# Kernel optimization log

Measured on AMD Instinct MI355X. Metric: run time of the kernel, lower is better.

The kernel has to match this reference:

```python
import jax, jax.numpy as jnp
import numpy as np

B, S, D = 2, 2048, 2560
H, HKV, HD = 8, 4, 256
EPS = 1e-6
SCALING = 256 ** -0.5          # query_pre_attn_scalar ** -0.5
SOFTCAP = 4096.0               # sliding_window passed positionally into softcap slot
NEG = -1e9


def rms_norm(x, w):
    # x: [..., HD]; computed in fp32 like the torch module
    xf = x.astype(jnp.float32)
    out = xf * jax.lax.rsqrt(jnp.mean(xf * xf, axis=-1, keepdims=True) + EPS)
    return (out * (1.0 + w.astype(jnp.float32))).astype(x.dtype)


def rotate_half(x):
    x1, x2 = x[..., : HD // 2], x[..., HD // 2:]
    return jnp.concatenate((-x2, x1), axis=-1)


def apply_rope(x, cos, sin):
    # cos/sin: [B, S, HD] -> broadcast over head axis 1
    c, s = cos[:, None], sin[:, None]
    return x * c + rotate_half(x) * s


def setup_inputs() -> dict:
    key = jax.random.key(0)
    ks = jax.random.split(key, 6)
    x = jax.random.normal(ks[0], (B, S, D), dtype=jnp.float32)
    # RoPE angles (theta=10000, linear scaling factor 8)
    inv_freq = 1.0 / (10000.0 ** (np.arange(0, HD, 2, dtype=np.float32) / HD))
    pos = np.arange(S, dtype=np.float32) / 8.0
    ang = np.einsum('s,d->sd', pos, inv_freq)
    ang = np.concatenate([ang, ang], axis=-1)               # [S, HD]
    cos = jnp.asarray(np.broadcast_to(np.cos(ang), (B, S, HD)).copy())
    sin = jnp.asarray(np.broadcast_to(np.sin(ang), (B, S, HD)).copy())
    # causal additive mask [B, 1, S, S]
    causal = np.where(np.tril(np.ones((S, S), dtype=bool)), 0.0, NEG).astype(np.float32)
    mask = jnp.asarray(np.broadcast_to(causal, (B, 1, S, S)).copy())
    sc = 0.02
    q_w = jax.random.normal(ks[1], (H * HD, D), dtype=jnp.float32) * sc
    k_w = jax.random.normal(ks[2], (HKV * HD, D), dtype=jnp.float32) * sc
    v_w = jax.random.normal(ks[3], (HKV * HD, D), dtype=jnp.float32) * sc
    o_w = jax.random.normal(ks[4], (D, H * HD), dtype=jnp.float32) * sc
    qn_w = jnp.zeros((HD,), dtype=jnp.float32)
    kn_w = jnp.zeros((HD,), dtype=jnp.float32)
    return {"x": x, "cos": cos, "sin": sin, "mask": mask,
            "q_w": q_w, "k_w": k_w, "v_w": v_w, "o_w": o_w,
            "qn_w": qn_w, "kn_w": kn_w}


def reference(x, cos, sin, mask, q_w, k_w, v_w, o_w, qn_w, kn_w):
    b, s, _ = x.shape
    # projections -> [B, H(kv), S, HD]
    q = (x @ q_w.T).reshape(b, s, H, HD).transpose(0, 2, 1, 3)
    k = (x @ k_w.T).reshape(b, s, HKV, HD).transpose(0, 2, 1, 3)
    v = (x @ v_w.T).reshape(b, s, HKV, HD).transpose(0, 2, 1, 3)
    q = rms_norm(q, qn_w)
    k = rms_norm(k, kn_w)
    q = apply_rope(q, cos, sin)
    k = apply_rope(k, cos, sin)
    # GQA: repeat kv heads (interleave matches repeat_interleave on dim=1)
    rep = H // HKV
    k = jnp.repeat(k, rep, axis=1)
    v = jnp.repeat(v, rep, axis=1)
    w = jnp.einsum('bhqd,bhkd->bhqk', q, k) * SCALING
    w = jnp.tanh(w / SOFTCAP) * SOFTCAP                     # softcap (bug-faithful)
    w = w + mask[:, :, :, : k.shape[2]]
    p = jax.nn.softmax(w.astype(jnp.float32), axis=-1).astype(q.dtype)
    attn = jnp.einsum('bhqk,bhkd->bhqd', p, v)
    attn = attn.transpose(0, 2, 1, 3).reshape(b, s, H * HD)
    return attn @ o_w.T
```

## Files before the change

### kernel.cpp

```cpp
#include <hip/hip_runtime.h>
#include <hip/hip_bf16.h>

#define BB   2
#define SS   2048
#define DD   2560
#define HH   8
#define HKVV 4
#define HDD  256
#define MM   (BB*SS)
#define NQ   (HH*HDD)
#define NKV  (HKVV*HDD)
#define SCALING 0.0625f
#define SOFTCAP 4096.0f
#define CAPC    (1.0f/(3.0f*SOFTCAP*SOFTCAP))
#define M0      20.0f

typedef __attribute__((ext_vector_type(8))) short short8;
typedef __attribute__((ext_vector_type(8))) unsigned short ushort8;
typedef __attribute__((ext_vector_type(4))) unsigned short us4;
typedef __attribute__((ext_vector_type(4))) float f32x4;

__device__ __forceinline__ float bf2f(unsigned short u) {
    union { unsigned int i; float f; } v; v.i = ((unsigned int)u) << 16; return v.f;
}
__device__ __forceinline__ unsigned short f2bf(float f) {
    union { float f; unsigned int i; } v; v.f = f;
    return (unsigned short)((v.i + 0x7fffu + ((v.i >> 16) & 1u)) >> 16);
}
__device__ __forceinline__ f32x4 mfma16(short8 a, short8 b, f32x4 c) {
    return __builtin_amdgcn_mfma_f32_16x16x32_bf16(a, b, c, 0, 0, 0);
}

__device__ __forceinline__ void async_cp16(const void* g, void* l) {
    __builtin_amdgcn_global_load_lds(
        (__attribute__((address_space(1))) void*)(g),
        (__attribute__((address_space(3))) void*)(l), 16, 0, 0);
}

__device__ __forceinline__ ushort8 ld8(const unsigned short* p) { return *(const ushort8*)p; }
__device__ __forceinline__ ushort8 ld8(const float* p) {
    ushort8 r;
#pragma unroll
    for (int i = 0; i < 8; i++) r[i] = f2bf(p[i]);
    return r;
}
__device__ __forceinline__ void stc(float* p, float v)          { *p = v; }
__device__ __forceinline__ void stc(unsigned short* p, float v) { *p = f2bf(v); }
__device__ __forceinline__ void stage8(const unsigned short* src, unsigned short* lds) {
    async_cp16(src, lds);
}
__device__ __forceinline__ void stage8(const float* src, unsigned short* lds) {
    *(ushort8*)lds = ld8(src);
}

__global__ __launch_bounds__(256) void cvt_bf16(const float* __restrict__ in,
                                                unsigned short* __restrict__ out, int n4)
{
    int i = blockIdx.x * 256 + threadIdx.x;
    const int stride = gridDim.x * 256;
    for (; i < n4; i += stride) {
        float4 v = ((const float4*)in)[i];
        us4 o;
        o[0] = f2bf(v.x); o[1] = f2bf(v.y); o[2] = f2bf(v.z); o[3] = f2bf(v.w);
        ((us4*)out)[i] = o;
    }
}

template<typename TA, typename TB, typename TC, bool VT_OUT>
__global__ __launch_bounds__(256) void gemm_k(const TA* __restrict__ A,
                                              const TB* __restrict__ Bm,
                                              TC* __restrict__ C,
                                              int M, int N, int K)
{
    __shared__ __align__(16) unsigned short As[128][32];
    __shared__ __align__(16) unsigned short Bs[128][32];

    const int tid  = threadIdx.x;
    const int bm   = blockIdx.x, bn = blockIdx.y;
    const int wave = tid >> 6, lane = tid & 63;
    const int quad = lane >> 4, lm = lane & 15;
    const int wm = (wave >> 1) * 64, wn = (wave & 1) * 64;

    f32x4 acc[4][4];
#pragma unroll
    for (int i = 0; i < 4; i++)
#pragma unroll
        for (int j = 0; j < 4; j++) acc[i][j] = (f32x4)0.0f;

    unsigned short* AsF = &As[0][0];
    unsigned short* BsF = &Bs[0][0];
    const int grow = tid >> 2;
    const int gcol = (tid & 3) * 8;
    const TA* Ab = A  + (size_t)(bm * 128) * K;
    const TB* Bb = Bm + (size_t)(bn * 128) * K;

    for (int k0 = 0; k0 < K; k0 += 32) {
        stage8(&Ab[(size_t)(grow     ) * K + k0 + gcol], AsF + tid * 8);
        stage8(&Ab[(size_t)(grow + 64) * K + k0 + gcol], AsF + 2048 + tid * 8);
        stage8(&Bb[(size_t)(grow     ) * K + k0 + gcol], BsF + tid * 8);
        stage8(&Bb[(size_t)(grow + 64) * K + k0 + gcol], BsF + 2048 + tid * 8);
        __syncthreads();

        short8 af[4], bf[4];
#pragma unroll
        for (int t = 0; t < 4; t++) af[t] = *(const short8*)&As[wm + t * 16 + lm][quad * 8];
#pragma unroll
        for (int t = 0; t < 4; t++) bf[t] = *(const short8*)&Bs[wn + t * 16 + lm][quad * 8];
#pragma unroll
        for (int i = 0; i < 4; i++)
#pragma unroll
            for (int j = 0; j < 4; j++)
                acc[i][j] = mfma16(af[i], bf[j], acc[i][j]);
        __syncthreads();
    }

#pragma unroll
    for (int i = 0; i < 4; i++)
#pragma unroll
        for (int j = 0; j < 4; j++) {
            if constexpr (VT_OUT) {
                int row0 = bm * 128 + wm + i * 16 + quad * 4;
                int col  = bn * 128 + wn + j * 16 + lm;
                int b    = row0 >> 11, s0 = row0 & (SS - 1);
                int kvh  = col >> 8,   d  = col & (HDD - 1);
                us4 pk;
#pragma unroll
                for (int r = 0; r < 4; r++) pk[r] = f2bf(acc[i][j][r]);
                *(us4*)&C[(((size_t)b * HKVV + kvh) * HDD + d) * SS + s0] = pk;
            } else {
#pragma unroll
                for (int r = 0; r < 4; r++) {
                    int row = bm * 128 + wm + i * 16 + quad * 4 + r;
                    int col = bn * 128 + wn + j * 16 + lm;
                    stc(&C[(size_t)row * N + col], acc[i][j][r]);
                }
            }
        }
}

__global__ __launch_bounds__(256) void norm_rope(unsigned short* __restrict__ X,
                                                 const float* __restrict__ nw,
                                                 const float* __restrict__ cosb,
                                                 const float* __restrict__ sinb,
                                                 int nheads)
{
    const int bs = blockIdx.x;
    const int h  = blockIdx.y;
    const int t  = threadIdx.x;

    __shared__ float xs[256];
    __shared__ float red[4];

    const size_t base = ((size_t)bs * nheads + h) * HDD;
    float v = bf2f(X[base + t]);
    xs[t] = v;

    float p = v * v;
#pragma unroll
    for (int off = 32; off >= 1; off >>= 1) p += __shfl_xor(p, off);
    if ((t & 63) == 0) red[t >> 6] = p;
    __syncthreads();
    float sum = red[0] + red[1] + red[2] + red[3];
    float rs  = rsqrtf(sum * (1.0f / HDD) + 1e-6f);

    const int pt = (t + 128) & 255;
    float w1 = 1.0f + nw[t];
    float w2 = 1.0f + nw[pt];
    float normed  = v * rs * w1;
    float partner = xs[pt] * rs * w2;
    float rot = (t < 128) ? -partner : partner;
    float c = cosb[(size_t)bs * HDD + t];
    float s = sinb[(size_t)bs * HDD + t];
    X[base + t] = f2bf(normed * c + rot * s);
}

__device__ const unsigned char unit_tbl[48] = {
    62, 124, 125, 120, 121,
    58, 116, 117, 112, 113,
    54, 108, 109, 104, 105,
    50, 100, 101,  96,  97,
    46,  92,  93,  88,  89,
    42,  84,  85,  80,  81,
    38,  76,  77,  72,  73,
    34,  68,  69,  64,  65,
    30,  26,  22,  18,  14, 10, 6, 2
};

__global__ __launch_bounds__(256) void attn_split(const unsigned short* __restrict__ Q,
                                                  const unsigned short* __restrict__ K,
                                                  const unsigned short* __restrict__ VT,
                                                  unsigned short* __restrict__ O,
                                                  float* __restrict__ Opart,
                                                  float* __restrict__ lpart)
{
    const int tid = threadIdx.x, w = tid >> 6, lane = tid & 63;
    const int quad = lane >> 4, lm = lane & 15;
    const int hb = blockIdx.x;
    const int h = hb & 7, b = hb >> 3, kvh = h >> 1;

    const unsigned int u = unit_tbl[blockIdx.y];
    const int qb = u >> 2;
    const bool single = (u & 2) != 0;
    const int half = u & 1;
    const int q0 = qb * 64;
    const int T  = 2 * (qb + 1);
    const int t_lo = (!single && half) ? (qb + 1) : 0;
    const int t_hi = single ? T : (half ? T : (qb + 1));

    __shared__ __align__(16) unsigned short Ks[2][32 * 256];
    __shared__ __align__(16) unsigned short Vt[2][256 * 32];
    __shared__ __align__(16) unsigned short Ps[4 * 512];

    const unsigned short* Qb = Q + (((size_t)b * SS + q0 + w * 16 + lm) * HH + h) * HDD;
    short8 qf[8];
#pragma unroll
    for (int c = 0; c < 8; c++) qf[c] = *(const short8*)&Qb[c * 32 + quad * 8];

    const unsigned short* Kb = K  + (size_t)b * SS * NKV + (size_t)kvh * HDD;
    const unsigned short* Vb = VT + ((size_t)b * HKVV + kvh) * HDD * (size_t)SS;

    f32x4 o_acc[16];
#pragma unroll
    for (int i = 0; i < 16; i++) o_acc[i] = (f32x4)0.0f;
    float l_r[4] = {0.f, 0.f, 0.f, 0.f};

    const int mylo = q0 + w * 16;
    const int row  = mylo + quad * 4;

    auto STAGE = [&](int bi, int k0) {
#pragma unroll
        for (int p = 0; p < 4; p++) {
            const int slot = p * 256 + tid;
            const int krow = slot >> 5, kc = slot & 31;
            async_cp16(&Kb[(size_t)(k0 + krow) * NKV + ((kc ^ (krow & 7)) * 8)],
                       &Ks[bi][slot * 8]);
            const int vd = slot >> 2, vc = slot & 3;
            async_cp16(&Vb[(size_t)vd * SS + k0 + ((vc ^ ((vd >> 1) & 3)) * 8)],
                       &Vt[bi][slot * 8]);
        }
    };

    STAGE(0, t_lo * 32);
    int cur = 0;

    for (int t = t_lo; t < t_hi; t++) {
        const int k0 = t * 32;

        if (t + 1 < t_hi) {
            STAGE(cur ^ 1, k0 + 32);
            asm volatile("s_waitcnt vmcnt(8)" ::: "memory");
        } else {
            asm volatile("s_waitcnt vmcnt(0)" ::: "memory");
        }
        __builtin_amdgcn_s_barrier();
        __builtin_amdgcn_sched_barrier(0);

        if (k0 <= mylo + 15) {
            f32x4 sa0 = (f32x4)0.0f, sa1 = (f32x4)0.0f;
            __builtin_amdgcn_s_setprio(1);
#pragma unroll
            for (int c = 0; c < 8; c++) {
                const int cs = (((c * 4 + quad) ^ (lm & 7))) * 8;
                short8 kf0 = *(const short8*)&Ks[cur][lm * 256 + cs];
                short8 kf1 = *(const short8*)&Ks[cur][(16 + lm) * 256 + cs];
                sa0 = mfma16(qf[c], kf0, sa0);
                sa1 = mfma16(qf[c], kf1, sa1);
            }
            __builtin_amdgcn_s_setprio(0);

            const bool msk = (k0 + 31 > mylo);
            float pe[2][4];
#pragma unroll
            for (int t2 = 0; t2 < 2; t2++) {
                const int key = k0 + t2 * 16 + lm;
#pragma unroll
                for (int r = 0; r < 4; r++) {
                    float s = (t2 ? sa1[r] : sa0[r]) * SCALING;
                    s = s - s * s * s * CAPC;
                    float e = __expf(s - M0);
                    if (msk && key > row + r) e = 0.0f;
                    pe[t2][r] = e;
                    l_r[r] += e;
                }
            }

#pragma unroll
            for (int t2 = 0; t2 < 2; t2++)
#pragma unroll
                for (int r = 0; r < 4; r++) {
                    const int g = (t2 * 2 + (lm >> 3)) ^ r ^ quad;
                    Ps[w * 512 + (quad * 4 + r) * 32 + g * 8 + (lm & 7)] = f2bf(pe[t2][r]);
                }
            asm volatile("s_waitcnt lgkmcnt(0)" ::: "memory");
            __builtin_amdgcn_sched_barrier(0);
            const int gr = quad ^ (lm & 3) ^ (lm >> 2);
            short8 pf = *(const short8*)&Ps[w * 512 + lm * 32 + gr * 8];

            __builtin_amdgcn_s_setprio(1);
#pragma unroll
            for (int nt = 0; nt < 16; nt++) {
                short8 vf = *(const short8*)&Vt[cur][(nt * 16 + lm) * 32
                                                    + ((quad ^ ((lm >> 1) & 3)) * 8)];
                o_acc[nt] = mfma16(pf, vf, o_acc[nt]);
            }
            __builtin_amdgcn_s_setprio(0);
        }

        __builtin_amdgcn_sched_barrier(0);
        __builtin_amdgcn_s_barrier();
        __builtin_amdgcn_sched_barrier(0);
        cur ^= 1;
    }

#pragma unroll
    for (int off = 1; off < 16; off <<= 1)
#pragma unroll
        for (int r = 0; r < 4; r++) l_r[r] += __shfl_xor(l_r[r], off);

    if (single) {
#pragma unroll
        for (int r = 0; r < 4; r++) {
            float inv = 1.0f / l_r[r];
            unsigned short* Ob = O + ((size_t)b * SS + row + r) * NQ + h * HDD;
#pragma unroll
            for (int nt = 0; nt < 16; nt++)
                Ob[nt * 16 + lm] = f2bf(o_acc[nt][r] * inv);
        }
    } else {
        const int slot = (((b * HH + h) * 16 + (qb - 16)) << 1) | half;
        float* Ob = Opart + ((size_t)slot * 64 + w * 16 + quad * 4) * 256;
#pragma unroll
        for (int r = 0; r < 4; r++) {
            if (lm == 0) lpart[slot * 64 + w * 16 + quad * 4 + r] = l_r[r];
#pragma unroll
            for (int nt = 0; nt < 16; nt++)
                Ob[(size_t)r * 256 + nt * 16 + lm] = o_acc[nt][r];
        }
    }
}

__global__ __launch_bounds__(256) void attn_reduce(const float* __restrict__ Op,
                                                   const float* __restrict__ lp,
                                                   unsigned short* __restrict__ ATT)
{
    const int sp  = blockIdx.x >> 4;
    const int wr0 = (blockIdx.x & 15) * 4;
    const int r   = threadIdx.x >> 6;
    const int c0  = (threadIdx.x & 63) * 4;
    const int wrow = wr0 + r;
    const int qbm = sp & 15, h = (sp >> 4) & 7, b = sp >> 7;

    const size_t base0 = ((size_t)(sp * 2) * 64 + wrow) * 256;
    const size_t base1 = base0 + (size_t)64 * 256;
    float4 a = *(const float4*)&Op[base0 + c0];
    float4 d = *(const float4*)&Op[base1 + c0];
    float l = lp[sp * 2 * 64 + wrow] + lp[(sp * 2 + 1) * 64 + wrow];
    float inv = 1.0f / l;
    us4 o;
    o[0] = f2bf((a.x + d.x) * inv); o[1] = f2bf((a.y + d.y) * inv);
    o[2] = f2bf((a.z + d.z) * inv); o[3] = f2bf((a.w + d.w) * inv);
    const int srow = (16 + qbm) * 64 + wrow;
    *(us4*)&ATT[(((size_t)b * SS + srow) * HH + h) * HDD + c0] = o;
}

__global__ __launch_bounds__(256) void attn_kernel(const unsigned short* __restrict__ Q,
                                                   const unsigned short* __restrict__ K,
                                                   const unsigned short* __restrict__ VT,
                                                   unsigned short* __restrict__ O)
{
    const int tid = threadIdx.x, w = tid >> 6, lane = tid & 63;
    const int quad = lane >> 4, lm = lane & 15;
    const int h = blockIdx.y, b = blockIdx.z, kvh = h >> 1;

    const int bx = blockIdx.x;
    const int qb = (bx & 1) ? (31 - (bx >> 1)) : (bx >> 1);
    const int q0 = qb * 64;
    const int T  = 2 * (qb + 1);

    __shared__ __align__(16) unsigned short Ks[2][32 * 256];
    __shared__ __align__(16) unsigned short Vt[2][256 * 32];
    __shared__ __align__(16) unsigned short Ps[4 * 512];

    const unsigned short* Qb = Q + (((size_t)b * SS + q0 + w * 16 + lm) * HH + h) * HDD;
    short8 qf[8];
#pragma unroll
    for (int c = 0; c < 8; c++) qf[c] = *(const short8*)&Qb[c * 32 + quad * 8];

    const unsigned short* Kb = K  + (size_t)b * SS * NKV + (size_t)kvh * HDD;
    const unsigned short* Vb = VT + ((size_t)b * HKVV + kvh) * HDD * (size_t)SS;

    f32x4 o_acc[16];
#pragma unroll
    for (int i = 0; i < 16; i++) o_acc[i] = (f32x4)0.0f;
    float l_r[4] = {0.f, 0.f, 0.f, 0.f};

    const int mylo = q0 + w * 16;
    const int row  = mylo + quad * 4;

    auto STAGE = [&](int bi, int k0) {
#pragma unroll
        for (int p = 0; p < 4; p++) {
            const int slot = p * 256 + tid;
            const int krow = slot >> 5, kc = slot & 31;
            async_cp16(&Kb[(size_t)(k0 + krow) * NKV + ((kc ^ (krow & 7)) * 8)],
                       &Ks[bi][slot * 8]);
            const int vd = slot >> 2, vc = slot & 3;
            async_cp16(&Vb[(size_t)vd * SS + k0 + ((vc ^ ((vd >> 1) & 3)) * 8)],
                       &Vt[bi][slot * 8]);
        }
    };

    STAGE(0, 0);
    int cur = 0;

    for (int t = 0; t < T; t++) {
        const int k0 = t * 32;

        if (t + 1 < T) {
            STAGE(cur ^ 1, k0 + 32);
            asm volatile("s_waitcnt vmcnt(8)" ::: "memory");
        } else {
            asm volatile("s_waitcnt vmcnt(0)" ::: "memory");
        }
        __builtin_amdgcn_s_barrier();
        __builtin_amdgcn_sched_barrier(0);

        if (k0 <= mylo + 15) {
            f32x4 sa0 = (f32x4)0.0f, sa1 = (f32x4)0.0f;
            __builtin_amdgcn_s_setprio(1);
#pragma unroll
            for (int c = 0; c < 8; c++) {
                const int cs = (((c * 4 + quad) ^ (lm & 7))) * 8;
                short8 kf0 = *(const short8*)&Ks[cur][lm * 256 + cs];
                short8 kf1 = *(const short8*)&Ks[cur][(16 + lm) * 256 + cs];
                sa0 = mfma16(qf[c], kf0, sa0);
                sa1 = mfma16(qf[c], kf1, sa1);
            }
            __builtin_amdgcn_s_setprio(0);

            const bool msk = (k0 + 31 > mylo);
            float pe[2][4];
#pragma unroll
            for (int t2 = 0; t2 < 2; t2++) {
                const int key = k0 + t2 * 16 + lm;
#pragma unroll
                for (int r = 0; r < 4; r++) {
                    float s = (t2 ? sa1[r] : sa0[r]) * SCALING;
                    s = s - s * s * s * CAPC;
                    float e = __expf(s - M0);
                    if (msk && key > row + r) e = 0.0f;
                    pe[t2][r] = e;
                    l_r[r] += e;
                }
            }

#pragma unroll
            for (int t2 = 0; t2 < 2; t2++)
#pragma unroll
                for (int r = 0; r < 4; r++) {
                    const int g = (t2 * 2 + (lm >> 3)) ^ r ^ quad;
                    Ps[w * 512 + (quad * 4 + r) * 32 + g * 8 + (lm & 7)] = f2bf(pe[t2][r]);
                }
            asm volatile("s_waitcnt lgkmcnt(0)" ::: "memory");
            __builtin_amdgcn_sched_barrier(0);
            const int gr = quad ^ (lm & 3) ^ (lm >> 2);
            short8 pf = *(const short8*)&Ps[w * 512 + lm * 32 + gr * 8];

            __builtin_amdgcn_s_setprio(1);
#pragma unroll
            for (int nt = 0; nt < 16; nt++) {
                short8 vf = *(const short8*)&Vt[cur][(nt * 16 + lm) * 32
                                                    + ((quad ^ ((lm >> 1) & 3)) * 8)];
                o_acc[nt] = mfma16(pf, vf, o_acc[nt]);
            }
            __builtin_amdgcn_s_setprio(0);
        }

        __builtin_amdgcn_sched_barrier(0);
        __builtin_amdgcn_s_barrier();
        __builtin_amdgcn_sched_barrier(0);
        cur ^= 1;
    }

#pragma unroll
    for (int off = 1; off < 16; off <<= 1)
#pragma unroll
        for (int r = 0; r < 4; r++) l_r[r] += __shfl_xor(l_r[r], off);
#pragma unroll
    for (int r = 0; r < 4; r++) {
        float inv = 1.0f / l_r[r];
        unsigned short* Ob = O + ((size_t)b * SS + row + r) * NQ + h * HDD;
#pragma unroll
        for (int nt = 0; nt < 16; nt++)
            Ob[nt * 16 + lm] = f2bf(o_acc[nt][r] * inv);
    }
}

extern "C" void kernel_launch(void* const* d_in, const int* in_sizes, int n_in,
                              void* d_out, int out_size, void* d_ws, size_t ws_size,
                              hipStream_t stream)
{
    const float* x    = (const float*)d_in[0];
    const float* cosb = (const float*)d_in[1];
    const float* sinb = (const float*)d_in[2];
    const float* q_w  = (const float*)d_in[4];
    const float* k_w  = (const float*)d_in[5];
    const float* v_w  = (const float*)d_in[6];
    const float* o_w  = (const float*)d_in[7];
    const float* qn_w = (const float*)d_in[8];
    const float* kn_w = (const float*)d_in[9];
    float* out = (float*)d_out;

    const size_t sz_xb = (size_t)MM * DD;
    const size_t sz_wq = (size_t)NQ * DD;
    const size_t sz_wk = (size_t)NKV * DD;
    const size_t sz_q  = (size_t)MM * NQ;
    const size_t sz_k  = (size_t)MM * NKV;

    const size_t needA = (sz_xb + 2 * sz_wq + 2 * sz_wk + sz_q + 2 * sz_k) * 2;
    const size_t needB = (2 * sz_wq + 2 * sz_wk + sz_q + 2 * sz_k) * 2;

    if (ws_size >= needA) {
        unsigned short* xb  = (unsigned short*)d_ws;
        unsigned short* wqb = xb  + sz_xb;
        unsigned short* wkb = wqb + sz_wq;
        unsigned short* wvb = wkb + sz_wk;
        unsigned short* wob = wvb + sz_wk;
        unsigned short* Qw  = wob + sz_wq;
        unsigned short* Kw  = Qw  + sz_q;
        unsigned short* VTw = Kw  + sz_k;
        float* Opart = (float*)d_ws;
        float* lpart = Opart + (size_t)512 * 64 * 256;
        unsigned short* ATT = Qw;

        cvt_bf16<<<2048, 256, 0, stream>>>(x,   xb,  (int)(sz_xb / 4));
        cvt_bf16<<<2048, 256, 0, stream>>>(q_w, wqb, (int)(sz_wq / 4));
        cvt_bf16<<<1024, 256, 0, stream>>>(k_w, wkb, (int)(sz_wk / 4));
        cvt_bf16<<<1024, 256, 0, stream>>>(v_w, wvb, (int)(sz_wk / 4));
        cvt_bf16<<<2048, 256, 0, stream>>>(o_w, wob, (int)(sz_wq / 4));

        gemm_k<unsigned short, unsigned short, unsigned short, false>
            <<<dim3(MM/128, NQ /128), 256, 0, stream>>>(xb, wqb, Qw,  MM, NQ,  DD);
        gemm_k<unsigned short, unsigned short, unsigned short, false>
            <<<dim3(MM/128, NKV/128), 256, 0, stream>>>(xb, wkb, Kw,  MM, NKV, DD);
        gemm_k<unsigned short, unsigned short, unsigned short, true>
            <<<dim3(MM/128, NKV/128), 256, 0, stream>>>(xb, wvb, VTw, MM, NKV, DD);

        norm_rope<<<dim3(MM, HH),   256, 0, stream>>>(Qw, qn_w, cosb, sinb, HH);
        norm_rope<<<dim3(MM, HKVV), 256, 0, stream>>>(Kw, kn_w, cosb, sinb, HKVV);

        attn_split<<<dim3(16, 48), 256, 0, stream>>>(Qw, Kw, VTw, ATT, Opart, lpart);
        attn_reduce<<<4096, 256, 0, stream>>>(Opart, lpart, ATT);

        gemm_k<unsigned short, unsigned short, float, false>
            <<<dim3(MM/128, DD/128), 256, 0, stream>>>(ATT, wob, out, MM, DD, NQ);
    } else if (ws_size >= needB) {
        unsigned short* wqb = (unsigned short*)d_ws;
        unsigned short* wkb = wqb + sz_wq;
        unsigned short* wvb = wkb + sz_wk;
        unsigned short* wob = wvb + sz_wk;
        unsigned short* Qw  = wob + sz_wq;
        unsigned short* Kw  = Qw  + sz_q;
        unsigned short* VTw = Kw  + sz_k;
        unsigned short* ATT = wqb;

        cvt_bf16<<<2048, 256, 0, stream>>>(q_w, wqb, (int)(sz_wq / 4));
        cvt_bf16<<<1024, 256, 0, stream>>>(k_w, wkb, (int)(sz_wk / 4));
        cvt_bf16<<<1024, 256, 0, stream>>>(v_w, wvb, (int)(sz_wk / 4));
        cvt_bf16<<<2048, 256, 0, stream>>>(o_w, wob, (int)(sz_wq / 4));

        gemm_k<float, unsigned short, unsigned short, false>
            <<<dim3(MM/128, NQ /128), 256, 0, stream>>>(x, wqb, Qw,  MM, NQ,  DD);
        gemm_k<float, unsigned short, unsigned short, false>
            <<<dim3(MM/128, NKV/128), 256, 0, stream>>>(x, wkb, Kw,  MM, NKV, DD);
        gemm_k<float, unsigned short, unsigned short, true>
            <<<dim3(MM/128, NKV/128), 256, 0, stream>>>(x, wvb, VTw, MM, NKV, DD);

        norm_rope<<<dim3(MM, HH),   256, 0, stream>>>(Qw, qn_w, cosb, sinb, HH);
        norm_rope<<<dim3(MM, HKVV), 256, 0, stream>>>(Kw, kn_w, cosb, sinb, HKVV);

        attn_kernel<<<dim3(32, HH, BB), 256, 0, stream>>>(Qw, Kw, VTw, ATT);

        gemm_k<unsigned short, unsigned short, float, false>
            <<<dim3(MM/128, DD/128), 256, 0, stream>>>(ATT, wob, out, MM, DD, NQ);
    } else {
        unsigned short* Qw  = (unsigned short*)d_ws;
        unsigned short* Kw  = Qw  + sz_q;
        unsigned short* VTw = Kw  + sz_k;
        unsigned short* ATT = VTw + sz_k;

        gemm_k<float, float, unsigned short, false>
            <<<dim3(MM/128, NQ /128), 256, 0, stream>>>(x, q_w, Qw,  MM, NQ,  DD);
        gemm_k<float, float, unsigned short, false>
            <<<dim3(MM/128, NKV/128), 256, 0, stream>>>(x, k_w, Kw,  MM, NKV, DD);
        gemm_k<float, float, unsigned short, true>
            <<<dim3(MM/128, NKV/128), 256, 0, stream>>>(x, v_w, VTw, MM, NKV, DD);

        norm_rope<<<dim3(MM, HH),   256, 0, stream>>>(Qw, qn_w, cosb, sinb, HH);
        norm_rope<<<dim3(MM, HKVV), 256, 0, stream>>>(Kw, kn_w, cosb, sinb, HKVV);

        attn_kernel<<<dim3(32, HH, BB), 256, 0, stream>>>(Qw, Kw, VTw, ATT);

        gemm_k<unsigned short, float, float, false>
            <<<dim3(MM/128, DD/128), 256, 0, stream>>>(ATT, o_w, out, MM, DD, NQ);
    }
}
```

Baseline: 549.8 us.

## Single-buffer V tile in attention LDS and split K/V staging with extra barrier

The V tile moves from a double buffer to a single LDS buffer, so the attention block uses less shared memory and may fit more resident blocks per CU. K keeps its prefetch one tile ahead. V for the next tile is now issued only after the PV MFMAs finish, so its load overlaps only with the next QK^T and softmax phase. A second vmcnt wait and barrier per iteration guard the single V buffer. This adds synchronisation and exposes more V load latency in exchange for the lower LDS footprint.

```diff
diff --git a/kernel.cpp b/kernel.cpp
--- a/kernel.cpp
+++ b/kernel.cpp
@@ -208,7 +208,7 @@
     const int t_hi = single ? T : (half ? T : (qb + 1));
 
     __shared__ __align__(16) unsigned short Ks[2][32 * 256];
-    __shared__ __align__(16) unsigned short Vt[2][256 * 32];
+    __shared__ __align__(16) unsigned short Vt[256 * 32];
     __shared__ __align__(16) unsigned short Ps[4 * 512];
 
     const unsigned short* Qb = Q + (((size_t)b * SS + q0 + w * 16 + lm) * HH + h) * HDD;
@@ -227,34 +227,43 @@
     const int mylo = q0 + w * 16;
     const int row  = mylo + quad * 4;
 
-    auto STAGE = [&](int bi, int k0) {
+    auto STAGE_K = [&](int bi, int k0) {
 #pragma unroll
         for (int p = 0; p < 4; p++) {
             const int slot = p * 256 + tid;
             const int krow = slot >> 5, kc = slot & 31;
             async_cp16(&Kb[(size_t)(k0 + krow) * NKV + ((kc ^ (krow & 7)) * 8)],
                        &Ks[bi][slot * 8]);
+        }
+    };
+    auto STAGE_V = [&](int k0) {
+#pragma unroll
+        for (int p = 0; p < 4; p++) {
+            const int slot = p * 256 + tid;
             const int vd = slot >> 2, vc = slot & 3;
             async_cp16(&Vb[(size_t)vd * SS + k0 + ((vc ^ ((vd >> 1) & 3)) * 8)],
-                       &Vt[bi][slot * 8]);
+                       &Vt[slot * 8]);
         }
     };
 
-    STAGE(0, t_lo * 32);
+    STAGE_K(0, t_lo * 32);
+    STAGE_V(t_lo * 32);
     int cur = 0;
 
     for (int t = t_lo; t < t_hi; t++) {
         const int k0 = t * 32;
-
-        if (t + 1 < t_hi) {
-            STAGE(cur ^ 1, k0 + 32);
+        const bool more = (t + 1 < t_hi);
+
+        if (more) {
+            STAGE_K(cur ^ 1, k0 + 32);
             asm volatile("s_waitcnt vmcnt(8)" ::: "memory");
         } else {
-            asm volatile("s_waitcnt vmcnt(0)" ::: "memory");
+            asm volatile("s_waitcnt vmcnt(4)" ::: "memory");
         }
         __builtin_amdgcn_s_barrier();
         __builtin_amdgcn_sched_barrier(0);
 
+        short8 pf;
         if (k0 <= mylo + 15) {
             f32x4 sa0 = (f32x4)0.0f, sa1 = (f32x4)0.0f;
             __builtin_amdgcn_s_setprio(1);
@@ -294,13 +303,20 @@
             asm volatile("s_waitcnt lgkmcnt(0)" ::: "memory");
             __builtin_amdgcn_sched_barrier(0);
             const int gr = quad ^ (lm & 3) ^ (lm >> 2);
-            short8 pf = *(const short8*)&Ps[w * 512 + lm * 32 + gr * 8];
-
+            pf = *(const short8*)&Ps[w * 512 + lm * 32 + gr * 8];
+        }
+
+        if (more) asm volatile("s_waitcnt vmcnt(4)" ::: "memory");
+        else      asm volatile("s_waitcnt vmcnt(0)" ::: "memory");
+        __builtin_amdgcn_s_barrier();
+        __builtin_amdgcn_sched_barrier(0);
+
+        if (k0 <= mylo + 15) {
             __builtin_amdgcn_s_setprio(1);
 #pragma unroll
             for (int nt = 0; nt < 16; nt++) {
-                short8 vf = *(const short8*)&Vt[cur][(nt * 16 + lm) * 32
-                                                    + ((quad ^ ((lm >> 1) & 3)) * 8)];
+                short8 vf = *(const short8*)&Vt[(nt * 16 + lm) * 32
+                                                + ((quad ^ ((lm >> 1) & 3)) * 8)];
                 o_acc[nt] = mfma16(pf, vf, o_acc[nt]);
             }
             __builtin_amdgcn_s_setprio(0);
@@ -309,6 +325,7 @@
         __builtin_amdgcn_sched_barrier(0);
         __builtin_amdgcn_s_barrier();
         __builtin_amdgcn_sched_barrier(0);
+        if (more) STAGE_V(k0 + 32);
         cur ^= 1;
     }
 
```

Measured after the change: 551.4 us. About the same (+0.3%).
